# Performance work log

Hardware: AMD Instinct MI355X
Metric: run time of the kernel (lower is better)

## Reference

```python
import jax, jax.numpy as jnp
import numpy as np

EPS = 1e-6

def elu_feature_map(x):
    return jax.nn.elu(x) + 1.0

def setup_inputs() -> dict:
    key = jax.random.key(0)
    k1, k2, k3 = jax.random.split(key, 3)
    N, S, H, D, M = 16, 4096, 16, 64, 64
    query = jax.random.normal(k1, (N, H, D), dtype=jnp.float32)
    keys = jax.random.normal(k2, (N, S, H, D), dtype=jnp.float32)
    values = jax.random.normal(k3, (N, S, H, M), dtype=jnp.float32)
    key_mask = jnp.ones((N, S), dtype=jnp.float32)  # key_lengths.float_matrix
    return {"query": query, "keys": keys, "values": values, "key_mask": key_mask}

def reference(query, keys, values, key_mask):
    # Q: [N,H,D]
    Q = elu_feature_map(query)
    # K: [N,S,H,D], masked over sequence
    K = elu_feature_map(keys) * key_mask[:, :, None, None]
    # S_state: [N,H,M,D] -- K^T V outer-product reduction over sequence
    S_state = jnp.einsum('nshd,nshm->nhmd', K, values)
    # Z: [N,H,D] -- normalizer
    Z = K.sum(axis=1)
    # QZ: [N,H]
    QZ = 1.0 / (jnp.einsum('nhd,nhd->nh', Q, Z) + EPS)
    # V_out: [N,H,M]
    V_out = jnp.einsum('nhd,nhmd,nh->nhm', Q, S_state, QZ)
    return (V_out, S_state, Z)
```

## Files before the change

### kernel.cpp

```cpp
#include <hip/hip_runtime.h>


#define S_LEN  4096
#define NHEAD  16
#define DDIM   64
#define MDIM   64
#define NWAVE  4
#define CH_S   32
#define NCHK   32
#define PITCH  1024

#define OUT_SOFF  (16 * 16 * 64)
#define OUT_ZOFF  (OUT_SOFF + 16 * 16 * 64 * 64)

using short8 = __attribute__((ext_vector_type(8))) short;
using f32x4  = __attribute__((ext_vector_type(4))) float;
using uint4v = __attribute__((ext_vector_type(4))) unsigned int;

union FragCast { uint4v u; short8 s; };

typedef const __attribute__((address_space(1))) void gvoid_t;
typedef __attribute__((address_space(3))) void lvoid_t;

#define GLOAD16(dst, src) \
    __builtin_amdgcn_global_load_lds((gvoid_t*)(src), (lvoid_t*)(dst), 16, 0, 0)
#define GLOAD4(dst, src) \
    __builtin_amdgcn_global_load_lds((gvoid_t*)(src), (lvoid_t*)(dst), 4, 0, 0)
#define WAITVM17 do { asm volatile("s_waitcnt vmcnt(17)" ::: "memory"); \
                      __builtin_amdgcn_sched_barrier(0); } while (0)
#define WAITVM0  do { asm volatile("s_waitcnt vmcnt(0)"  ::: "memory"); \
                      __builtin_amdgcn_sched_barrier(0); } while (0)

__device__ __forceinline__ float elup1(float x) {
    return x > 0.0f ? x + 1.0f : __expf(x);
}

__device__ __forceinline__ unsigned bfpack(float a, float b) {
    union { float f; unsigned u; } ca, cb;
    ca.f = a; cb.f = b;
    const unsigned ra = ca.u + 0x7FFFu + ((ca.u >> 16) & 1u);
    const unsigned rb = cb.u + 0x7FFFu + ((cb.u >> 16) & 1u);
    return (ra >> 16) | (rb & 0xFFFF0000u);
}

struct WaveBuf {
    float K[CH_S][DDIM];
    float V[CH_S][MDIM];
    float mk[64];
};

__global__ __launch_bounds__(256, 1)
void rcla_fused(const float* __restrict__ query,
                const float* __restrict__ keys,
                const float* __restrict__ values,
                const float* __restrict__ kmask,
                float* __restrict__ out)
{
    __shared__ WaveBuf hot[NWAVE][2];
    __shared__ float mbuf[64][68];
    __shared__ float zrows[NWAVE][64];
    __shared__ float qb[64];
    __shared__ float zb[64];

    const int t    = threadIdx.x;
    const int wave = t >> 6;
    const int lane = t & 63;
    const int c16  = lane & 15;
    const int g    = lane >> 4;
    const int pair = blockIdx.x;
    const int nIdx = pair >> 4;
    const int hIdx = pair & 15;

    const int sWave = wave * (NCHK * CH_S);
    const size_t base = ((size_t)nIdx * S_LEN + sWave) * PITCH
                      + (size_t)hIdx * DDIM;
    const int li = lane >> 4;
    const int ci = lane & 15;
    const float* kl = keys   + base + (size_t)li * PITCH + ci * 4;
    const float* vl = values + base + (size_t)li * PITCH + ci * 4;
    const float* ml = kmask + (size_t)nIdx * S_LEN + sWave + (lane & 31);

    f32x4 acc[4][4];
#pragma unroll
    for (int i = 0; i < 4; ++i)
#pragma unroll
        for (int j = 0; j < 4; ++j) acc[i][j] = f32x4{0.f, 0.f, 0.f, 0.f};
    float zz[4] = {0.f, 0.f, 0.f, 0.f};

    auto issue = [&](int p, int ch) {
        const size_t co = (size_t)ch * CH_S * PITCH;
        float* Kd = &hot[wave][p].K[0][0];
        float* Vd = &hot[wave][p].V[0][0];
#pragma unroll
        for (int r = 0; r < 8; ++r)
            GLOAD16(Kd + r * 256, kl + co + (size_t)r * 4 * PITCH);
#pragma unroll
        for (int r = 0; r < 8; ++r)
            GLOAD16(Vd + r * 256, vl + co + (size_t)r * 4 * PITCH);
        GLOAD4(&hot[wave][p].mk[0], ml + ch * CH_S);
    };

    auto compute = [&](int p) {
        const WaveBuf& B = hot[wave][p];
        float mk8[8];
#pragma unroll
        for (int j = 0; j < 8; ++j) mk8[j] = B.mk[g * 8 + j];
        float kraw[4][8], vraw[4][8];
#pragma unroll
        for (int tj = 0; tj < 4; ++tj)
#pragma unroll
            for (int j = 0; j < 8; ++j)
                kraw[tj][j] = B.K[g * 8 + j][tj * 16 + c16];
#pragma unroll
        for (int ti = 0; ti < 4; ++ti)
#pragma unroll
            for (int j = 0; j < 8; ++j)
                vraw[ti][j] = B.V[g * 8 + j][ti * 16 + c16];

        unsigned kf[4][4], vf[4][4];
#pragma unroll
        for (int tj = 0; tj < 4; ++tj)
#pragma unroll
            for (int q = 0; q < 4; ++q) {
                const float e0 = elup1(kraw[tj][2 * q])     * mk8[2 * q];
                const float e1 = elup1(kraw[tj][2 * q + 1]) * mk8[2 * q + 1];
                zz[tj] += e0 + e1;
                kf[tj][q] = bfpack(e0, e1);
            }
#pragma unroll
        for (int ti = 0; ti < 4; ++ti)
#pragma unroll
            for (int q = 0; q < 4; ++q)
                vf[ti][q] = bfpack(vraw[ti][2 * q], vraw[ti][2 * q + 1]);

#pragma unroll
        for (int ti = 0; ti < 4; ++ti) {
            FragCast fa;
            fa.u = uint4v{vf[ti][0], vf[ti][1], vf[ti][2], vf[ti][3]};
#pragma unroll
            for (int tj = 0; tj < 4; ++tj) {
                FragCast fb;
                fb.u = uint4v{kf[tj][0], kf[tj][1], kf[tj][2], kf[tj][3]};
                acc[ti][tj] = __builtin_amdgcn_mfma_f32_16x16x32_bf16(
                    fa.s, fb.s, acc[ti][tj], 0, 0, 0);
            }
        }
    };

    issue(0, 0);
#pragma unroll 1
    for (int c = 0; c < NCHK - 2; c += 2) {
        issue(1, c + 1);
        WAITVM17;
        compute(0);
        issue(0, c + 2);
        WAITVM17;
        compute(1);
    }
    issue(1, NCHK - 1);
    WAITVM17;
    compute(0);
    WAITVM0;
    compute(1);

#pragma unroll
    for (int tj = 0; tj < 4; ++tj) {
        zz[tj] += __shfl_xor(zz[tj], 16, 64);
        zz[tj] += __shfl_xor(zz[tj], 32, 64);
    }

    __syncthreads();

    for (int rr = 0; rr < 4; ++rr) {
        if (wave == rr) {
#pragma unroll
            for (int ti = 0; ti < 4; ++ti)
#pragma unroll
                for (int tj = 0; tj < 4; ++tj)
#pragma unroll
                    for (int r = 0; r < 4; ++r) {
                        const int m = ti * 16 + g * 4 + r;
                        const int d = tj * 16 + c16;
                        if (rr == 0) mbuf[m][d]  = acc[ti][tj][r];
                        else         mbuf[m][d] += acc[ti][tj][r];
                    }
        }
        __syncthreads();
    }

    if (g == 0) {
#pragma unroll
        for (int tj = 0; tj < 4; ++tj)
            zrows[wave][tj * 16 + c16] = zz[tj];
    }
    if (t < 64) qb[t] = elup1(query[(size_t)pair * DDIM + t]);

    {
        const int m  = t >> 2;
        const int dc = (t & 3) * 16;
#pragma unroll
        for (int j = 0; j < 16; j += 4)
            *(float4*)&out[OUT_SOFF + (size_t)pair * 4096 + m * 64 + dc + j] =
                *(const float4*)&mbuf[m][dc + j];
    }
    __syncthreads();

    if (t < 64) {
        const float zv = zrows[0][t] + zrows[1][t] + zrows[2][t] + zrows[3][t];
        out[OUT_ZOFF + (size_t)pair * 64 + t] = zv;
        zb[t] = zv;
    }
    __syncthreads();

    if (wave == 0) {
        float zp = qb[lane] * zb[lane];
#pragma unroll
        for (int off = 32; off >= 1; off >>= 1) zp += __shfl_xor(zp, off, 64);
        const float qz = 1.0f / (zp + 1e-6f);
        float vs = 0.0f;
#pragma unroll
        for (int d = 0; d < 64; d += 4) {
            const float4 sv = *(const float4*)&mbuf[lane][d];
            vs = fmaf(qb[d],     sv.x, vs);
            vs = fmaf(qb[d + 1], sv.y, vs);
            vs = fmaf(qb[d + 2], sv.z, vs);
            vs = fmaf(qb[d + 3], sv.w, vs);
        }
        out[(size_t)pair * MDIM + lane] = qz * vs;
    }
}

extern "C" void kernel_launch(void* const* d_in, const int* in_sizes, int n_in,
                              void* d_out, int out_size, void* d_ws, size_t ws_size,
                              hipStream_t stream) {
    const float* q  = (const float*)d_in[0];
    const float* k  = (const float*)d_in[1];
    const float* v  = (const float*)d_in[2];
    const float* km = (const float*)d_in[3];
    float* out = (float*)d_out;
    rcla_fused<<<dim3(256), dim3(256), 0, stream>>>(q, k, v, km, out);
}
```

Baseline: 106.3 us.

## Double waves per block with half-size chunks, merging two chunks per MFMA

Raises the block to 8 waves, each streaming 16-row chunks instead of 32, so twice as many waves issue loads and hide memory latency within each (n,h) block. Each chunk is converted into half of a bf16 fragment, and the MFMA batch runs once per pair of chunks, keeping the 32-wide K dimension. Wait counts, the cross-wave reduction loop and the output store mapping are adjusted to match. The cost is a longer serial reduction of accumulators across 8 waves, more LDS use, and fewer bytes in flight per wave.

```diff
diff --git a/kernel.cpp b/kernel.cpp
--- a/kernel.cpp
+++ b/kernel.cpp
@@ -5,8 +5,8 @@
 #define NHEAD  16
 #define DDIM   64
 #define MDIM   64
-#define NWAVE  4
-#define CH_S   32
+#define NWAVE  8
+#define CH_S   16
 #define NCHK   32
 #define PITCH  1024
 
@@ -26,10 +26,8 @@
     __builtin_amdgcn_global_load_lds((gvoid_t*)(src), (lvoid_t*)(dst), 16, 0, 0)
 #define GLOAD4(dst, src) \
     __builtin_amdgcn_global_load_lds((gvoid_t*)(src), (lvoid_t*)(dst), 4, 0, 0)
-#define WAITVM17 do { asm volatile("s_waitcnt vmcnt(17)" ::: "memory"); \
-                      __builtin_amdgcn_sched_barrier(0); } while (0)
-#define WAITVM0  do { asm volatile("s_waitcnt vmcnt(0)"  ::: "memory"); \
-                      __builtin_amdgcn_sched_barrier(0); } while (0)
+#define WAITVM(N) do { asm volatile("s_waitcnt vmcnt(" #N ")" ::: "memory"); \
+                       __builtin_amdgcn_sched_barrier(0); } while (0)
 
 __device__ __forceinline__ float elup1(float x) {
     return x > 0.0f ? x + 1.0f : __expf(x);
@@ -43,20 +41,16 @@
     return (ra >> 16) | (rb & 0xFFFF0000u);
 }
 
-struct WaveBuf {
-    float K[CH_S][DDIM];
-    float V[CH_S][MDIM];
-    float mk[64];
-};
-
-__global__ __launch_bounds__(256, 1)
+__global__ __launch_bounds__(512, 1)
 void rcla_fused(const float* __restrict__ query,
                 const float* __restrict__ keys,
                 const float* __restrict__ values,
                 const float* __restrict__ kmask,
                 float* __restrict__ out)
 {
-    __shared__ WaveBuf hot[NWAVE][2];
+    __shared__ float Kbuf[NWAVE][2][CH_S * DDIM];
+    __shared__ float Vbuf[NWAVE][2][CH_S * DDIM];
+    __shared__ float mkb[NWAVE][2][64];
     __shared__ float mbuf[64][68];
     __shared__ float zrows[NWAVE][64];
     __shared__ float qb[64];
@@ -78,7 +72,7 @@
     const int ci = lane & 15;
     const float* kl = keys   + base + (size_t)li * PITCH + ci * 4;
     const float* vl = values + base + (size_t)li * PITCH + ci * 4;
-    const float* ml = kmask + (size_t)nIdx * S_LEN + sWave + (lane & 31);
+    const float* ml = kmask + (size_t)nIdx * S_LEN + sWave + (lane & 15);
 
     f32x4 acc[4][4];
 #pragma unroll
@@ -86,53 +80,54 @@
 #pragma unroll
         for (int j = 0; j < 4; ++j) acc[i][j] = f32x4{0.f, 0.f, 0.f, 0.f};
     float zz[4] = {0.f, 0.f, 0.f, 0.f};
-
-    auto issue = [&](int p, int ch) {
+    unsigned kf[4][4], vf[4][4];
+
+    auto issue = [&](int b, int ch) {
         const size_t co = (size_t)ch * CH_S * PITCH;
-        float* Kd = &hot[wave][p].K[0][0];
-        float* Vd = &hot[wave][p].V[0][0];
-#pragma unroll
-        for (int r = 0; r < 8; ++r)
+        float* Kd = &Kbuf[wave][0][0] + b * (CH_S * DDIM);
+        float* Vd = &Vbuf[wave][0][0] + b * (CH_S * DDIM);
+#pragma unroll
+        for (int r = 0; r < 4; ++r)
             GLOAD16(Kd + r * 256, kl + co + (size_t)r * 4 * PITCH);
 #pragma unroll
-        for (int r = 0; r < 8; ++r)
+        for (int r = 0; r < 4; ++r)
             GLOAD16(Vd + r * 256, vl + co + (size_t)r * 4 * PITCH);
-        GLOAD4(&hot[wave][p].mk[0], ml + ch * CH_S);
+        GLOAD4(&mkb[wave][b][0], ml + ch * CH_S);
     };
 
-    auto compute = [&](int p) {
-        const WaveBuf& B = hot[wave][p];
-        float mk8[8];
-#pragma unroll
-        for (int j = 0; j < 8; ++j) mk8[j] = B.mk[g * 8 + j];
-        float kraw[4][8], vraw[4][8];
-#pragma unroll
-        for (int tj = 0; tj < 4; ++tj)
-#pragma unroll
-            for (int j = 0; j < 8; ++j)
-                kraw[tj][j] = B.K[g * 8 + j][tj * 16 + c16];
-#pragma unroll
-        for (int ti = 0; ti < 4; ++ti)
-#pragma unroll
-            for (int j = 0; j < 8; ++j)
-                vraw[ti][j] = B.V[g * 8 + j][ti * 16 + c16];
-
-        unsigned kf[4][4], vf[4][4];
-#pragma unroll
-        for (int tj = 0; tj < 4; ++tj)
-#pragma unroll
-            for (int q = 0; q < 4; ++q) {
-                const float e0 = elup1(kraw[tj][2 * q])     * mk8[2 * q];
-                const float e1 = elup1(kraw[tj][2 * q + 1]) * mk8[2 * q + 1];
-                zz[tj] += e0 + e1;
-                kf[tj][q] = bfpack(e0, e1);
-            }
-#pragma unroll
-        for (int ti = 0; ti < 4; ++ti)
-#pragma unroll
-            for (int q = 0; q < 4; ++q)
-                vf[ti][q] = bfpack(vraw[ti][2 * q], vraw[ti][2 * q + 1]);
-
+    auto xform = [&](int b, int hf) {
+        const float* Kb = &Kbuf[wave][0][0] + b * (CH_S * DDIM);
+        const float* Vb = &Vbuf[wave][0][0] + b * (CH_S * DDIM);
+        const float* mk = &mkb[wave][b][0];
+        float m4[4];
+#pragma unroll
+        for (int j = 0; j < 4; ++j) m4[j] = mk[g * 4 + j];
+#pragma unroll
+        for (int tj = 0; tj < 4; ++tj) {
+            float kr[4];
+#pragma unroll
+            for (int j = 0; j < 4; ++j)
+                kr[j] = Kb[(g * 4 + j) * DDIM + tj * 16 + c16];
+            const float e0 = elup1(kr[0]) * m4[0];
+            const float e1 = elup1(kr[1]) * m4[1];
+            const float e2 = elup1(kr[2]) * m4[2];
+            const float e3 = elup1(kr[3]) * m4[3];
+            zz[tj] += (e0 + e1) + (e2 + e3);
+            kf[tj][2 * hf]     = bfpack(e0, e1);
+            kf[tj][2 * hf + 1] = bfpack(e2, e3);
+        }
+#pragma unroll
+        for (int ti = 0; ti < 4; ++ti) {
+            float vr[4];
+#pragma unroll
+            for (int j = 0; j < 4; ++j)
+                vr[j] = Vb[(g * 4 + j) * DDIM + ti * 16 + c16];
+            vf[ti][2 * hf]     = bfpack(vr[0], vr[1]);
+            vf[ti][2 * hf + 1] = bfpack(vr[2], vr[3]);
+        }
+    };
+
+    auto domfma = [&]() {
 #pragma unroll
         for (int ti = 0; ti < 4; ++ti) {
             FragCast fa;
@@ -151,17 +146,19 @@
 #pragma unroll 1
     for (int c = 0; c < NCHK - 2; c += 2) {
         issue(1, c + 1);
-        WAITVM17;
-        compute(0);
+        WAITVM(9);
+        xform(0, 0);
         issue(0, c + 2);
-        WAITVM17;
-        compute(1);
+        WAITVM(9);
+        xform(1, 1);
+        domfma();
     }
     issue(1, NCHK - 1);
-    WAITVM17;
-    compute(0);
-    WAITVM0;
-    compute(1);
+    WAITVM(9);
+    xform(0, 0);
+    WAITVM(0);
+    xform(1, 1);
+    domfma();
 
 #pragma unroll
     for (int tj = 0; tj < 4; ++tj) {
@@ -171,7 +168,7 @@
 
     __syncthreads();
 
-    for (int rr = 0; rr < 4; ++rr) {
+    for (int rr = 0; rr < NWAVE; ++rr) {
         if (wave == rr) {
 #pragma unroll
             for (int ti = 0; ti < 4; ++ti)
@@ -196,17 +193,19 @@
     if (t < 64) qb[t] = elup1(query[(size_t)pair * DDIM + t]);
 
     {
-        const int m  = t >> 2;
-        const int dc = (t & 3) * 16;
-#pragma unroll
-        for (int j = 0; j < 16; j += 4)
+        const int m  = t >> 3;
+        const int dc = (t & 7) * 8;
+#pragma unroll
+        for (int j = 0; j < 8; j += 4)
             *(float4*)&out[OUT_SOFF + (size_t)pair * 4096 + m * 64 + dc + j] =
                 *(const float4*)&mbuf[m][dc + j];
     }
     __syncthreads();
 
     if (t < 64) {
-        const float zv = zrows[0][t] + zrows[1][t] + zrows[2][t] + zrows[3][t];
+        float zv = 0.f;
+#pragma unroll
+        for (int r = 0; r < NWAVE; ++r) zv += zrows[r][t];
         out[OUT_ZOFF + (size_t)pair * 64 + t] = zv;
         zb[t] = zv;
     }
@@ -238,5 +237,5 @@
     const float* v  = (const float*)d_in[2];
     const float* km = (const float*)d_in[3];
     float* out = (float*)d_out;
-    rcla_fused<<<dim3(256), dim3(256), 0, stream>>>(q, k, v, km, out);
-}
+    rcla_fused<<<dim3(256), dim3(512), 0, stream>>>(q, k, v, km, out);
+}
```

After: 111.0 us. 4.4% more time.
